# Performance work log

Measured on AMD Instinct MI355X. Metric: run time of the kernel, lower is better.

Reference implementation:

```python
import jax, jax.numpy as jnp
import numpy as np

ALPHA = 0.2       # LeakyReLU negative slope
MASK_FILL = 1e-15 # value placed at non-edges before softmax (as in the original)
OUT_DIM = 64


def setup_inputs() -> dict:
    key = jax.random.key(0)
    k1, k2, k3, k4 = jax.random.split(key, 4)
    N, IN_DIM, D = 8192, 256, OUT_DIM
    h = jax.random.normal(k1, (N, IN_DIM), dtype=jnp.float32)
    # dense 0/1 adjacency (float, used only via A > 0)
    A = jax.random.randint(k2, (N, N), 0, 2).astype(jnp.float32)
    W = jax.random.normal(k3, (IN_DIM, D), dtype=jnp.float32) * (1.0 / np.sqrt(IN_DIM))
    a = jax.random.normal(k4, (2 * D,), dtype=jnp.float32) * (1.0 / np.sqrt(2 * D))
    return {"h": h, "A": A, "W": W, "a": a}


def reference(h, A, W, a):
    D = OUT_DIM
    Wh = h @ W                                   # [N, D]
    # attn([Wh_i || Wh_j]) == Wh_i . a[:D] + Wh_j . a[D:]  -- fused, avoids [N,N,2D]
    s_src = Wh @ a[:D]                           # [N]
    s_dst = Wh @ a[D:]                           # [N]
    e = jax.nn.leaky_relu(s_src[:, None] + s_dst[None, :], negative_slope=ALPHA)  # [N, N]
    attention = jnp.where(A > 0, e, MASK_FILL)
    attention = jax.nn.softmax(attention, axis=1)
    h_prime = attention @ Wh                     # [N, D]
    return jax.nn.elu(h_prime)                   # concat=True branch
```

## Files before the change

### kernel.cpp

```cpp
#include <hip/hip_runtime.h>
#include <hip/hip_bf16.h>

#define GAT_N 8192
#define GAT_K 256
#define GAT_D 64
#define GAT_ALPHA 0.2f
#define GAT_FILL 1e-15f

typedef float f32x4 __attribute__((ext_vector_type(4)));
typedef short bf16x8 __attribute__((ext_vector_type(8)));

static __device__ __forceinline__ unsigned f2bf_u(float x) {
  unsigned u = __float_as_uint(x);
  u += 0x7FFFu + ((u >> 16) & 1u);
  return u >> 16;
}

static __device__ __forceinline__ float rfl(float x) {
  return __uint_as_float(__builtin_amdgcn_readfirstlane(__float_as_uint(x)));
}

static __device__ __forceinline__ f32x4 ntload(const float* p) {
  return __builtin_nontemporal_load((const f32x4*)p);
}

__global__ __launch_bounds__(256) void k_prep(const float* __restrict__ h,
                                              const float* __restrict__ W,
                                              const float* __restrict__ av,
                                              float* __restrict__ s_src,
                                              float* __restrict__ s_dst,
                                              short* __restrict__ WhT,
                                              float* __restrict__ bmax) {
  __shared__ short T[4][64][8];
  __shared__ float wmLds[4];
  const int tid = threadIdx.x;
  const int wv = tid >> 6, lane = tid & 63;
  const int r0 = blockIdx.x * 32 + wv * 8;

  float acc[8], acc2[8];
#pragma unroll
  for (int r = 0; r < 8; ++r) { acc[r] = 0.f; acc2[r] = 0.f; }

  for (int kc = 0; kc < GAT_K; kc += 32) {
    float Wreg[32];
#pragma unroll
    for (int e = 0; e < 32; ++e) Wreg[e] = W[(size_t)(kc + e) * GAT_D + lane];
#pragma unroll
    for (int r = 0; r < 8; ++r) {
      const f32x4* h4 = (const f32x4*)(h + (size_t)(r0 + r) * GAT_K + kc);
#pragma unroll
      for (int q = 0; q < 8; ++q) {
        f32x4 hv = h4[q];
        acc[r] += hv[0] * Wreg[4 * q + 0];
        acc2[r] += hv[1] * Wreg[4 * q + 1];
        acc[r] += hv[2] * Wreg[4 * q + 2];
        acc2[r] += hv[3] * Wreg[4 * q + 3];
      }
    }
  }

  const float a_s = av[lane];
  const float a_d = av[64 + lane];
  float wmax = -3.0e38f;
#pragma unroll
  for (int r = 0; r < 8; ++r) {
    const float accf = acc[r] + acc2[r];
    T[wv][lane][r] = (short)f2bf_u(accf);
    float vs = accf * a_s, vd = accf * a_d;
#pragma unroll
    for (int off = 32; off > 0; off >>= 1) {
      vs += __shfl_xor(vs, off);
      vd += __shfl_xor(vd, off);
    }
    if (lane == 0) { s_src[r0 + r] = vs; s_dst[r0 + r] = vd; }
    wmax = fmaxf(wmax, vd);
  }
  bf16x8 vt = *(const bf16x8*)&T[wv][lane][0];
  *(bf16x8*)(WhT + (size_t)lane * GAT_N + r0) = vt;

  if (lane == 0) wmLds[wv] = wmax;
  __syncthreads();
  if (tid == 0) {
    bmax[blockIdx.x] = fmaxf(fmaxf(wmLds[0], wmLds[1]), fmaxf(wmLds[2], wmLds[3]));
  }
}

#define BM 16
#define JB 2048
#define NWAVE 8

__global__ __launch_bounds__(512, 4) void k_attn(
    const float* __restrict__ A,
    const float* __restrict__ s_src,
    const float* __restrict__ s_dst,
    const short* __restrict__ WhT,
    const float* __restrict__ bmax,
    float* __restrict__ out) {
  __shared__ char smem[65536];

  const int tid = threadIdx.x;
  const int wv = tid >> 6, lane = tid & 63;
  const int rsub = lane & 15, kg = lane >> 4;
  const int i0 = blockIdx.x * BM;

  float bm = fmaxf(fmaxf(bmax[lane], bmax[lane + 64]),
                   fmaxf(bmax[lane + 128], bmax[lane + 192]));
#pragma unroll
  for (int off = 32; off > 0; off >>= 1) bm = fmaxf(bm, __shfl_xor(bm, off));
  const float tmax = bm;

  float si_[BM], mh_[BM];
#pragma unroll
  for (int r = 0; r < BM; ++r) {
    float s = s_src[i0 + r];
    float x0 = s + tmax;
    float m = fmaxf(fmaxf(x0, GAT_ALPHA * x0), GAT_FILL);
    si_[r] = rfl(s);
    mh_[r] = rfl(m);
  }

  bf16x8 ones;
#pragma unroll
  for (int e = 0; e < 8; ++e) ones[e] = (short)0x3F80;

  f32x4 acc0 = {0.f, 0.f, 0.f, 0.f};
  f32x4 acc1 = {0.f, 0.f, 0.f, 0.f};
  f32x4 acc2 = {0.f, 0.f, 0.f, 0.f};
  f32x4 acc3 = {0.f, 0.f, 0.f, 0.f};
  f32x4 accl = {0.f, 0.f, 0.f, 0.f};

  const short* pb0 = WhT + (size_t)(0 * 16 + rsub) * GAT_N;
  const short* pb1 = WhT + (size_t)(1 * 16 + rsub) * GAT_N;
  const short* pb2 = WhT + (size_t)(2 * 16 + rsub) * GAT_N;
  const short* pb3 = WhT + (size_t)(3 * 16 + rsub) * GAT_N;

  for (int chunk = 0; chunk < GAT_N / JB; ++chunk) {
    const int jc = chunk * JB;
    const f32x4 tj = *(const f32x4*)(s_dst + jc + tid * 4);
    const float* Abase = A + (size_t)i0 * GAT_N + jc + tid * 4;

    f32x4 a_cur = ntload(Abase);
#pragma unroll
    for (int r = 0; r < BM; ++r) {
      f32x4 a_nxt;
      if (r < BM - 1) a_nxt = ntload(Abase + (size_t)(r + 1) * GAT_N);
      const float si = si_[r], mh = mh_[r];
      unsigned pk[4];
#pragma unroll
      for (int e = 0; e < 4; ++e) {
        float x = si + tj[e];
        float v = fmaxf(x, GAT_ALPHA * x);
        v = (a_cur[e] > 0.f) ? v : GAT_FILL;
        pk[e] = f2bf_u(__expf(v - mh));
      }
      uint2 w;
      w.x = pk[0] | (pk[1] << 16);
      w.y = pk[2] | (pk[3] << 16);
      *(uint2*)(&smem[(r << 12) + ((tid << 3) ^ ((r & 7) << 4))]) = w;
      a_cur = a_nxt;
    }
    __syncthreads();

#pragma unroll
    for (int kq = 0; kq < 8; ++kq) {
      const int cb = (wv << 9) + (kq << 6) + (kg << 4);
      bf16x8 af = *(const bf16x8*)(&smem[(rsub << 12) + (cb ^ ((rsub & 7) << 4))]);
      const int bcol = jc + (wv << 8) + (kq << 5) + (kg << 3);
      bf16x8 b0 = *(const bf16x8*)(pb0 + bcol);
      bf16x8 b1 = *(const bf16x8*)(pb1 + bcol);
      bf16x8 b2 = *(const bf16x8*)(pb2 + bcol);
      bf16x8 b3 = *(const bf16x8*)(pb3 + bcol);
      acc0 = __builtin_amdgcn_mfma_f32_16x16x32_bf16(af, b0, acc0, 0, 0, 0);
      acc1 = __builtin_amdgcn_mfma_f32_16x16x32_bf16(af, b1, acc1, 0, 0, 0);
      acc2 = __builtin_amdgcn_mfma_f32_16x16x32_bf16(af, b2, acc2, 0, 0, 0);
      acc3 = __builtin_amdgcn_mfma_f32_16x16x32_bf16(af, b3, acc3, 0, 0, 0);
      accl = __builtin_amdgcn_mfma_f32_16x16x32_bf16(af, ones, accl, 0, 0, 0);
    }
    __syncthreads();
  }

  float* lds_o = (float*)smem;
  float* lds_l = (float*)(smem + 32768);
#pragma unroll
  for (int r = 0; r < 4; ++r) {
    const int orow = kg * 4 + r;
    lds_o[wv * 1024 + orow * 64 + 0 * 16 + rsub] = acc0[r];
    lds_o[wv * 1024 + orow * 64 + 1 * 16 + rsub] = acc1[r];
    lds_o[wv * 1024 + orow * 64 + 2 * 16 + rsub] = acc2[r];
    lds_o[wv * 1024 + orow * 64 + 3 * 16 + rsub] = acc3[r];
    if (rsub == 0) lds_l[wv * 16 + orow] = accl[r];
  }
  __syncthreads();

  for (int idx = tid; idx < BM * GAT_D; idx += 512) {
    const int r = idx >> 6, c = idx & 63;
    float o = 0.f, ll = 0.f;
#pragma unroll
    for (int w = 0; w < NWAVE; ++w) {
      o += lds_o[w * 1024 + r * 64 + c];
      ll += lds_l[w * 16 + r];
    }
    float val = o / ll;
    out[(size_t)(i0 + r) * GAT_D + c] = (val > 0.f) ? val : (__expf(val) - 1.f);
  }
}

extern "C" void kernel_launch(void* const* d_in, const int* in_sizes, int n_in,
                              void* d_out, int out_size, void* d_ws, size_t ws_size,
                              hipStream_t stream) {
  const float* h = (const float*)d_in[0];
  const float* A = (const float*)d_in[1];
  const float* W = (const float*)d_in[2];
  const float* a = (const float*)d_in[3];
  float* out = (float*)d_out;

  const size_t need = 69632 + (size_t)GAT_D * GAT_N * 2;
  if (ws_size < need) return;
  float* bmax = (float*)d_ws;
  float* s_src = (float*)((char*)d_ws + 4096);
  float* s_dst = (float*)((char*)d_ws + 36864);
  short* WhT = (short*)((char*)d_ws + 69632);

  k_prep<<<dim3(256), dim3(256), 0, stream>>>(h, W, a, s_src, s_dst, WhT, bmax);
  k_attn<<<dim3(GAT_N / BM), dim3(512), 0, stream>>>(A, s_src, s_dst, WhT, bmax, out);
}
```

Before: 133.6 us.

## Prefetch adjacency rows per wave across chunks and precompute exp offsets

```diff
diff --git a/kernel.cpp b/kernel.cpp
--- a/kernel.cpp
+++ b/kernel.cpp
@@ -102,6 +102,20 @@
   const int wv = tid >> 6, lane = tid & 63;
   const int rsub = lane & 15, kg = lane >> 4;
   const int i0 = blockIdx.x * BM;
+  const int r0 = wv * 2, r1 = wv * 2 + 1;
+
+  const float* A0 = A + (size_t)(i0 + r0) * GAT_N + lane * 4;
+  const float* A1 = A + (size_t)(i0 + r1) * GAT_N + lane * 4;
+
+  f32x4 Ra[2][4], Rb[2][4];
+  auto issue = [&](int b, int jcol) {
+#pragma unroll
+    for (int s = 0; s < 4; ++s) {
+      Ra[b][s] = ntload(A0 + jcol + s * 256);
+      Rb[b][s] = ntload(A1 + jcol + s * 256);
+    }
+  };
+  issue(0, 0);
 
   float bm = fmaxf(fmaxf(bmax[lane], bmax[lane + 64]),
                    fmaxf(bmax[lane + 128], bmax[lane + 192]));
@@ -109,14 +123,22 @@
   for (int off = 32; off > 0; off >>= 1) bm = fmaxf(bm, __shfl_xor(bm, off));
   const float tmax = bm;
 
-  float si_[BM], mh_[BM];
-#pragma unroll
-  for (int r = 0; r < BM; ++r) {
-    float s = s_src[i0 + r];
-    float x0 = s + tmax;
+  const float sA = s_src[i0 + r0];
+  const float sB = s_src[i0 + r1];
+  float e1a, e2a, ca, e1b, e2b, cb;
+  {
+    float x0 = sA + tmax;
     float m = fmaxf(fmaxf(x0, GAT_ALPHA * x0), GAT_FILL);
-    si_[r] = rfl(s);
-    mh_[r] = rfl(m);
+    e1a = rfl(sA - m);
+    e2a = rfl(GAT_ALPHA * sA - m);
+    ca = rfl(__expf(GAT_FILL - m));
+  }
+  {
+    float x0 = sB + tmax;
+    float m = fmaxf(fmaxf(x0, GAT_ALPHA * x0), GAT_FILL);
+    e1b = rfl(sB - m);
+    e2b = rfl(GAT_ALPHA * sB - m);
+    cb = rfl(__expf(GAT_FILL - m));
   }
 
   bf16x8 ones;
@@ -134,37 +156,44 @@
   const short* pb2 = WhT + (size_t)(2 * 16 + rsub) * GAT_N;
   const short* pb3 = WhT + (size_t)(3 * 16 + rsub) * GAT_N;
 
+  auto stage_row = [&](int r, f32x4 av, f32x4 t, float e1, float e2, float cc,
+                       int sg) {
+    unsigned pk[4];
+#pragma unroll
+    for (int e = 0; e < 4; ++e) {
+      float arg = fmaxf(t[e] + e1, fmaf(GAT_ALPHA, t[e], e2));
+      float pe = __expf(arg);
+      pe = (av[e] > 0.f) ? pe : cc;
+      pk[e] = f2bf_u(pe);
+    }
+    uint2 w;
+    w.x = pk[0] | (pk[1] << 16);
+    w.y = pk[2] | (pk[3] << 16);
+    *(uint2*)(&smem[(r << 12) + (((sg << 9) | (lane << 3)) ^ ((r & 7) << 4))]) = w;
+  };
+
+  auto stage_half = [&](int b, int jc, int half) {
+#pragma unroll
+    for (int s = 0; s < 4; ++s) {
+      const int sg = half * 4 + s;
+      const f32x4 t = *(const f32x4*)(s_dst + jc + sg * 256 + lane * 4);
+      stage_row(r0, Ra[b][s], t, e1a, e2a, ca, sg);
+      stage_row(r1, Rb[b][s], t, e1b, e2b, cb, sg);
+    }
+  };
+
   for (int chunk = 0; chunk < GAT_N / JB; ++chunk) {
     const int jc = chunk * JB;
-    const f32x4 tj = *(const f32x4*)(s_dst + jc + tid * 4);
-    const float* Abase = A + (size_t)i0 * GAT_N + jc + tid * 4;
-
-    f32x4 a_cur = ntload(Abase);
-#pragma unroll
-    for (int r = 0; r < BM; ++r) {
-      f32x4 a_nxt;
-      if (r < BM - 1) a_nxt = ntload(Abase + (size_t)(r + 1) * GAT_N);
-      const float si = si_[r], mh = mh_[r];
-      unsigned pk[4];
-#pragma unroll
-      for (int e = 0; e < 4; ++e) {
-        float x = si + tj[e];
-        float v = fmaxf(x, GAT_ALPHA * x);
-        v = (a_cur[e] > 0.f) ? v : GAT_FILL;
-        pk[e] = f2bf_u(__expf(v - mh));
-      }
-      uint2 w;
-      w.x = pk[0] | (pk[1] << 16);
-      w.y = pk[2] | (pk[3] << 16);
-      *(uint2*)(&smem[(r << 12) + ((tid << 3) ^ ((r & 7) << 4))]) = w;
-      a_cur = a_nxt;
-    }
+    issue(1, jc + 1024);
+    stage_half(0, jc, 0);
+    if (chunk < 3) issue(0, jc + JB);
+    stage_half(1, jc, 1);
     __syncthreads();
 
 #pragma unroll
     for (int kq = 0; kq < 8; ++kq) {
-      const int cb = (wv << 9) + (kq << 6) + (kg << 4);
-      bf16x8 af = *(const bf16x8*)(&smem[(rsub << 12) + (cb ^ ((rsub & 7) << 4))]);
+      const int cbyte = (wv << 9) + (kq << 6) + (kg << 4);
+      bf16x8 af = *(const bf16x8*)(&smem[(rsub << 12) + (cbyte ^ ((rsub & 7) << 4))]);
       const int bcol = jc + (wv << 8) + (kq << 5) + (kg << 3);
       bf16x8 b0 = *(const bf16x8*)(pb0 + bcol);
       bf16x8 b1 = *(const bf16x8*)(pb1 + bcol);
```

After: 160.5 us. +20.1%, slower.

## Compress adjacency into bitmask in fused prep kernel, select via cndmask in attention

Applied to the files above, without the earlier changes.

```diff
diff --git a/kernel.cpp b/kernel.cpp
--- a/kernel.cpp
+++ b/kernel.cpp
@@ -9,6 +9,7 @@
 
 typedef float f32x4 __attribute__((ext_vector_type(4)));
 typedef short bf16x8 __attribute__((ext_vector_type(8)));
+typedef short bf16x4 __attribute__((ext_vector_type(4)));
 
 static __device__ __forceinline__ unsigned f2bf_u(float x) {
   unsigned u = __float_as_uint(x);
@@ -20,33 +21,61 @@
   return __uint_as_float(__builtin_amdgcn_readfirstlane(__float_as_uint(x)));
 }
 
-static __device__ __forceinline__ f32x4 ntload(const float* p) {
-  return __builtin_nontemporal_load((const f32x4*)p);
-}
-
-__global__ __launch_bounds__(256) void k_prep(const float* __restrict__ h,
-                                              const float* __restrict__ W,
-                                              const float* __restrict__ av,
-                                              float* __restrict__ s_src,
-                                              float* __restrict__ s_dst,
-                                              short* __restrict__ WhT,
-                                              float* __restrict__ bmax) {
-  __shared__ short T[4][64][8];
-  __shared__ float wmLds[4];
+static __device__ __forceinline__ float bitsel(unsigned long long w, float pe,
+                                               float cc) {
+  float res;
+  asm("v_cndmask_b32 %0, %1, %2, %3" : "=v"(res) : "v"(cc), "v"(pe), "s"(w));
+  return res;
+}
+
+#define PREP_BLOCKS 512
+#define CMP_BLOCKS 2048
+
+__global__ __launch_bounds__(256) void k0_fused(
+    const float* __restrict__ A, const float* __restrict__ h,
+    const float* __restrict__ W, const float* __restrict__ av,
+    unsigned long long* __restrict__ mask, float* __restrict__ s_src,
+    float* __restrict__ s_dst, short* __restrict__ WhT,
+    float* __restrict__ bmax) {
   const int tid = threadIdx.x;
   const int wv = tid >> 6, lane = tid & 63;
-  const int r0 = blockIdx.x * 32 + wv * 8;
-
-  float acc[8], acc2[8];
-#pragma unroll
-  for (int r = 0; r < 8; ++r) { acc[r] = 0.f; acc2[r] = 0.f; }
+
+  if (blockIdx.x >= PREP_BLOCKS) {
+    const int row = (blockIdx.x - PREP_BLOCKS) * 4 + wv;
+    const float* p = A + (size_t)row * GAT_N + lane * 4;
+    unsigned long long* mrow = mask + (size_t)row * 128;
+    f32x4 cur = __builtin_nontemporal_load((const f32x4*)p);
+#pragma unroll 4
+    for (int g = 0; g < 32; ++g) {
+      f32x4 nxt;
+      if (g < 31)
+        nxt = __builtin_nontemporal_load((const f32x4*)(p + (g + 1) * 256));
+      unsigned long long b0 = __ballot(cur[0] > 0.f);
+      unsigned long long b1 = __ballot(cur[1] > 0.f);
+      unsigned long long b2 = __ballot(cur[2] > 0.f);
+      unsigned long long b3 = __ballot(cur[3] > 0.f);
+      if (lane < 4) {
+        unsigned long long w = (lane == 0) ? b0 : (lane == 1) ? b1 : (lane == 2) ? b2 : b3;
+        mrow[g * 4 + lane] = w;
+      }
+      cur = nxt;
+    }
+    return;
+  }
+
+  __shared__ float wmLds[4];
+  const int r0 = blockIdx.x * 16 + wv * 4;
+
+  float acc[4], acc2[4];
+#pragma unroll
+  for (int r = 0; r < 4; ++r) { acc[r] = 0.f; acc2[r] = 0.f; }
 
   for (int kc = 0; kc < GAT_K; kc += 32) {
     float Wreg[32];
 #pragma unroll
     for (int e = 0; e < 32; ++e) Wreg[e] = W[(size_t)(kc + e) * GAT_D + lane];
 #pragma unroll
-    for (int r = 0; r < 8; ++r) {
+    for (int r = 0; r < 4; ++r) {
       const f32x4* h4 = (const f32x4*)(h + (size_t)(r0 + r) * GAT_K + kc);
 #pragma unroll
       for (int q = 0; q < 8; ++q) {
@@ -62,10 +91,11 @@
   const float a_s = av[lane];
   const float a_d = av[64 + lane];
   float wmax = -3.0e38f;
-#pragma unroll
-  for (int r = 0; r < 8; ++r) {
+  bf16x4 vt;
+#pragma unroll
+  for (int r = 0; r < 4; ++r) {
     const float accf = acc[r] + acc2[r];
-    T[wv][lane][r] = (short)f2bf_u(accf);
+    vt[r] = (short)f2bf_u(accf);
     float vs = accf * a_s, vd = accf * a_d;
 #pragma unroll
     for (int off = 32; off > 0; off >>= 1) {
@@ -75,8 +105,7 @@
     if (lane == 0) { s_src[r0 + r] = vs; s_dst[r0 + r] = vd; }
     wmax = fmaxf(wmax, vd);
   }
-  bf16x8 vt = *(const bf16x8*)&T[wv][lane][0];
-  *(bf16x8*)(WhT + (size_t)lane * GAT_N + r0) = vt;
+  *(bf16x4*)(WhT + (size_t)lane * GAT_N + r0) = vt;
 
   if (lane == 0) wmLds[wv] = wmax;
   __syncthreads();
@@ -90,7 +119,7 @@
 #define NWAVE 8
 
 __global__ __launch_bounds__(512, 4) void k_attn(
-    const float* __restrict__ A,
+    const unsigned long long* __restrict__ mask,
     const float* __restrict__ s_src,
     const float* __restrict__ s_dst,
     const short* __restrict__ WhT,
@@ -100,23 +129,26 @@
 
   const int tid = threadIdx.x;
   const int wv = tid >> 6, lane = tid & 63;
+  const int wvu = __builtin_amdgcn_readfirstlane(wv);
   const int rsub = lane & 15, kg = lane >> 4;
   const int i0 = blockIdx.x * BM;
 
-  float bm = fmaxf(fmaxf(bmax[lane], bmax[lane + 64]),
-                   fmaxf(bmax[lane + 128], bmax[lane + 192]));
+  float bm = -3.0e38f;
+#pragma unroll
+  for (int k = 0; k < 8; ++k) bm = fmaxf(bm, bmax[lane + 64 * k]);
 #pragma unroll
   for (int off = 32; off > 0; off >>= 1) bm = fmaxf(bm, __shfl_xor(bm, off));
   const float tmax = bm;
 
-  float si_[BM], mh_[BM];
+  float e1_[BM], e2_[BM], c_[BM];
 #pragma unroll
   for (int r = 0; r < BM; ++r) {
     float s = s_src[i0 + r];
     float x0 = s + tmax;
     float m = fmaxf(fmaxf(x0, GAT_ALPHA * x0), GAT_FILL);
-    si_[r] = rfl(s);
-    mh_[r] = rfl(m);
+    e1_[r] = rfl(s - m);
+    e2_[r] = rfl(GAT_ALPHA * s - m);
+    c_[r] = rfl(__expf(GAT_FILL - m));
   }
 
   bf16x8 ones;
@@ -136,35 +168,42 @@
 
   for (int chunk = 0; chunk < GAT_N / JB; ++chunk) {
     const int jc = chunk * JB;
-    const f32x4 tj = *(const f32x4*)(s_dst + jc + tid * 4);
-    const float* Abase = A + (size_t)i0 * GAT_N + jc + tid * 4;
-
-    f32x4 a_cur = ntload(Abase);
+    const f32x4 t = *(const f32x4*)(s_dst + jc + tid * 4);
+
 #pragma unroll
     for (int r = 0; r < BM; ++r) {
-      f32x4 a_nxt;
-      if (r < BM - 1) a_nxt = ntload(Abase + (size_t)(r + 1) * GAT_N);
-      const float si = si_[r], mh = mh_[r];
+      const unsigned long long* mw =
+          mask + (size_t)(i0 + r) * 128 + (size_t)(chunk * 8 + wvu) * 4;
+      unsigned long long w0 = mw[0], w1 = mw[1], w2 = mw[2], w3 = mw[3];
+      const float e1 = e1_[r], e2 = e2_[r], cc = c_[r];
       unsigned pk[4];
-#pragma unroll
-      for (int e = 0; e < 4; ++e) {
-        float x = si + tj[e];
-        float v = fmaxf(x, GAT_ALPHA * x);
-        v = (a_cur[e] > 0.f) ? v : GAT_FILL;
-        pk[e] = f2bf_u(__expf(v - mh));
+      {
+        float pe = __expf(fmaxf(t[0] + e1, fmaf(GAT_ALPHA, t[0], e2)));
+        pk[0] = f2bf_u(bitsel(w0, pe, cc));
+      }
+      {
+        float pe = __expf(fmaxf(t[1] + e1, fmaf(GAT_ALPHA, t[1], e2)));
+        pk[1] = f2bf_u(bitsel(w1, pe, cc));
+      }
+      {
+        float pe = __expf(fmaxf(t[2] + e1, fmaf(GAT_ALPHA, t[2], e2)));
+        pk[2] = f2bf_u(bitsel(w2, pe, cc));
+      }
+      {
+        float pe = __expf(fmaxf(t[3] + e1, fmaf(GAT_ALPHA, t[3], e2)));
+        pk[3] = f2bf_u(bitsel(w3, pe, cc));
       }
       uint2 w;
       w.x = pk[0] | (pk[1] << 16);
       w.y = pk[2] | (pk[3] << 16);
       *(uint2*)(&smem[(r << 12) + ((tid << 3) ^ ((r & 7) << 4))]) = w;
-      a_cur = a_nxt;
     }
     __syncthreads();
 
 #pragma unroll
     for (int kq = 0; kq < 8; ++kq) {
-      const int cb = (wv << 9) + (kq << 6) + (kg << 4);
-      bf16x8 af = *(const bf16x8*)(&smem[(rsub << 12) + (cb ^ ((rsub & 7) << 4))]);
+      const int cbyte = (wv << 9) + (kq << 6) + (kg << 4);
+      bf16x8 af = *(const bf16x8*)(&smem[(rsub << 12) + (cbyte ^ ((rsub & 7) << 4))]);
       const int bcol = jc + (wv << 8) + (kq << 5) + (kg << 3);
       bf16x8 b0 = *(const bf16x8*)(pb0 + bcol);
       bf16x8 b1 = *(const bf16x8*)(pb1 + bcol);
@@ -214,13 +253,16 @@
   const float* a = (const float*)d_in[3];
   float* out = (float*)d_out;
 
-  const size_t need = 69632 + (size_t)GAT_D * GAT_N * 2;
+  const size_t need = 1179648 + (size_t)GAT_N * 128 * 8;
   if (ws_size < need) return;
   float* bmax = (float*)d_ws;
   float* s_src = (float*)((char*)d_ws + 4096);
   float* s_dst = (float*)((char*)d_ws + 36864);
   short* WhT = (short*)((char*)d_ws + 69632);
-
-  k_prep<<<dim3(256), dim3(256), 0, stream>>>(h, W, a, s_src, s_dst, WhT, bmax);
-  k_attn<<<dim3(GAT_N / BM), dim3(512), 0, stream>>>(A, s_src, s_dst, WhT, bmax, out);
-}
+  unsigned long long* mask = (unsigned long long*)((char*)d_ws + 1179648);
+
+  k0_fused<<<dim3(PREP_BLOCKS + CMP_BLOCKS), dim3(256), 0, stream>>>(
+      A, h, W, a, mask, s_src, s_dst, WhT, bmax);
+  k_attn<<<dim3(GAT_N / BM), dim3(512), 0, stream>>>(mask, s_src, s_dst, WhT,
+                                                     bmax, out);
+}
```

New measurement: 161.6 us. 20.9% more time.

## Double-buffer P tiles in LDS and prefetch A across chunks with precomputed exp terms

Applied to the files above, without the earlier changes.

```diff
diff --git a/kernel.cpp b/kernel.cpp
--- a/kernel.cpp
+++ b/kernel.cpp
@@ -18,10 +18,6 @@
 
 static __device__ __forceinline__ float rfl(float x) {
   return __uint_as_float(__builtin_amdgcn_readfirstlane(__float_as_uint(x)));
-}
-
-static __device__ __forceinline__ f32x4 ntload(const float* p) {
-  return __builtin_nontemporal_load((const f32x4*)p);
 }
 
 __global__ __launch_bounds__(256) void k_prep(const float* __restrict__ h,
@@ -86,7 +82,8 @@
 }
 
 #define BM 16
-#define JB 2048
+#define JB 1024
+#define NCHUNK (GAT_N / JB)
 #define NWAVE 8
 
 __global__ __launch_bounds__(512, 4) void k_attn(
@@ -102,6 +99,8 @@
   const int wv = tid >> 6, lane = tid & 63;
   const int rsub = lane & 15, kg = lane >> 4;
   const int i0 = blockIdx.x * BM;
+  const int par = wv >> 2;
+  const int cth = tid & 255;
 
   float bm = fmaxf(fmaxf(bmax[lane], bmax[lane + 64]),
                    fmaxf(bmax[lane + 128], bmax[lane + 192]));
@@ -109,14 +108,15 @@
   for (int off = 32; off > 0; off >>= 1) bm = fmaxf(bm, __shfl_xor(bm, off));
   const float tmax = bm;
 
-  float si_[BM], mh_[BM];
-#pragma unroll
-  for (int r = 0; r < BM; ++r) {
-    float s = s_src[i0 + r];
-    float x0 = s + tmax;
+  float e1_[8], e2_[8], c_[8];
+#pragma unroll
+  for (int s = 0; s < 8; ++s) {
+    float sc = s_src[i0 + 2 * s + par];
+    float x0 = sc + tmax;
     float m = fmaxf(fmaxf(x0, GAT_ALPHA * x0), GAT_FILL);
-    si_[r] = rfl(s);
-    mh_[r] = rfl(m);
+    e1_[s] = rfl(sc - m);
+    e2_[s] = rfl(GAT_ALPHA * sc - m);
+    c_[s] = rfl(__expf(GAT_FILL - m));
   }
 
   bf16x8 ones;
@@ -134,38 +134,47 @@
   const short* pb2 = WhT + (size_t)(2 * 16 + rsub) * GAT_N;
   const short* pb3 = WhT + (size_t)(3 * 16 + rsub) * GAT_N;
 
-  for (int chunk = 0; chunk < GAT_N / JB; ++chunk) {
+  const float* Abase = A + (size_t)(i0 + par) * GAT_N + cth * 4;
+  auto aaddr = [&](int g) {
+    return Abase + (size_t)((g & 7) * 2) * GAT_N + (g >> 3) * JB;
+  };
+
+  f32x4 buf[4];
+#pragma unroll
+  for (int g = 0; g < 4; ++g) buf[g] = *(const f32x4*)aaddr(g);
+
+  for (int chunk = 0; chunk < NCHUNK; ++chunk) {
     const int jc = chunk * JB;
-    const f32x4 tj = *(const f32x4*)(s_dst + jc + tid * 4);
-    const float* Abase = A + (size_t)i0 * GAT_N + jc + tid * 4;
-
-    f32x4 a_cur = ntload(Abase);
-#pragma unroll
-    for (int r = 0; r < BM; ++r) {
-      f32x4 a_nxt;
-      if (r < BM - 1) a_nxt = ntload(Abase + (size_t)(r + 1) * GAT_N);
-      const float si = si_[r], mh = mh_[r];
+    const int tile = (chunk & 1) << 15;
+    const f32x4 t = *(const f32x4*)(s_dst + jc + cth * 4);
+
+#pragma unroll
+    for (int s = 0; s < 8; ++s) {
+      const int g = chunk * 8 + s;
+      f32x4 av = buf[g & 3];
+      if (g + 4 < 64) buf[(g + 4) & 3] = *(const f32x4*)aaddr(g + 4);
+      const float e1 = e1_[s], e2 = e2_[s], cc = c_[s];
       unsigned pk[4];
 #pragma unroll
       for (int e = 0; e < 4; ++e) {
-        float x = si + tj[e];
-        float v = fmaxf(x, GAT_ALPHA * x);
-        v = (a_cur[e] > 0.f) ? v : GAT_FILL;
-        pk[e] = f2bf_u(__expf(v - mh));
+        float arg = fmaxf(t[e] + e1, fmaf(GAT_ALPHA, t[e], e2));
+        float pe = __expf(arg);
+        pe = (av[e] > 0.f) ? pe : cc;
+        pk[e] = f2bf_u(pe);
       }
       uint2 w;
       w.x = pk[0] | (pk[1] << 16);
       w.y = pk[2] | (pk[3] << 16);
-      *(uint2*)(&smem[(r << 12) + ((tid << 3) ^ ((r & 7) << 4))]) = w;
-      a_cur = a_nxt;
+      const int row = 2 * s + par;
+      *(uint2*)(&smem[tile + (row << 11) + (((cth << 3)) ^ ((row & 7) << 4))]) = w;
     }
     __syncthreads();
 
 #pragma unroll
-    for (int kq = 0; kq < 8; ++kq) {
-      const int cb = (wv << 9) + (kq << 6) + (kg << 4);
-      bf16x8 af = *(const bf16x8*)(&smem[(rsub << 12) + (cb ^ ((rsub & 7) << 4))]);
-      const int bcol = jc + (wv << 8) + (kq << 5) + (kg << 3);
+    for (int kq = 0; kq < 4; ++kq) {
+      const int cbyte = (wv << 8) + (kq << 6) + (kg << 4);
+      bf16x8 af = *(const bf16x8*)(&smem[tile + (rsub << 11) + (cbyte ^ ((rsub & 7) << 4))]);
+      const int bcol = jc + (wv << 7) + (kq << 5) + (kg << 3);
       bf16x8 b0 = *(const bf16x8*)(pb0 + bcol);
       bf16x8 b1 = *(const bf16x8*)(pb1 + bcol);
       bf16x8 b2 = *(const bf16x8*)(pb2 + bcol);
@@ -176,8 +185,9 @@
       acc3 = __builtin_amdgcn_mfma_f32_16x16x32_bf16(af, b3, acc3, 0, 0, 0);
       accl = __builtin_amdgcn_mfma_f32_16x16x32_bf16(af, ones, accl, 0, 0, 0);
     }
-    __syncthreads();
-  }
+  }
+
+  __syncthreads();
 
   float* lds_o = (float*)smem;
   float* lds_l = (float*)(smem + 32768);
```

Result: slower. 136.7 us (+2.3%).
